# Performance work log

Measured on AMD Instinct MI355X. Metric: run time of the kernel, lower is better.

The kernel has to match this reference:

```python
import jax, jax.numpy as jnp
import numpy as np

B, DEC_T, ENC_T = 64, 128, 1024
H, ENC_D, ATTN, VOCAB = 512, 512, 512, 128


def setup_inputs() -> dict:
    key = jax.random.key(0)
    ks = jax.random.split(key, 12)
    s = 0.05
    return {
        "inputs": jax.random.randint(ks[0], (B, DEC_T), 0, 127),
        "encoder_outputs": jax.random.normal(ks[1], (B, ENC_T, ENC_D), jnp.float32),
        "embedding": jax.random.normal(ks[2], (VOCAB, H), jnp.float32) * s,
        "w_ih": jax.random.normal(ks[3], (3 * H, H + ENC_D), jnp.float32) * s,
        "w_hh": jax.random.normal(ks[4], (3 * H, H), jnp.float32) * s,
        "b_ih": jnp.zeros((3 * H,), jnp.float32),
        "b_hh": jnp.zeros((3 * H,), jnp.float32),
        "attn_wq": jax.random.normal(ks[5], (ATTN, H), jnp.float32) * s,
        "attn_wv": jax.random.normal(ks[6], (ATTN, ENC_D), jnp.float32) * s,
        "attn_conv_w": jax.random.normal(ks[7], (ATTN, 1, 3), jnp.float32) * s,
        "attn_conv_b": jnp.zeros((ATTN,), jnp.float32),
        "attn_bias": jnp.zeros((ATTN,), jnp.float32),
        "attn_v": jax.random.normal(ks[8], (ATTN,), jnp.float32) * s,
        "fc_w": jax.random.normal(ks[9], (VOCAB, H + ENC_D), jnp.float32) * s,
        "fc_b": jnp.zeros((VOCAB,), jnp.float32),
    }


def reference(inputs, encoder_outputs, embedding, w_ih, w_hh, b_ih, b_hh,
              attn_wq, attn_wv, attn_conv_w, attn_conv_b, attn_bias, attn_v,
              fc_w, fc_b):
    emb = embedding[inputs]  # (B, dec_T, H); no eos in inputs so filter is identity
    # precompute encoder value projection once (reused every step)
    enc_proj = jnp.einsum('bte,ae->bta', encoder_outputs, attn_wv)  # (B, enc_T, A)

    def gru_step(h, x):
        gi = x @ w_ih.T + b_ih  # (B, 3H)
        gh = h @ w_hh.T + b_hh
        r = jax.nn.sigmoid(gi[:, :H] + gh[:, :H])
        z = jax.nn.sigmoid(gi[:, H:2 * H] + gh[:, H:2 * H])
        n = jnp.tanh(gi[:, 2 * H:] + r * gh[:, 2 * H:])
        return (1.0 - z) * n + z * h

    def step(carry, x_t):
        h, context, attn_w = carry
        rnn_in = jnp.concatenate([x_t, context], axis=1)  # (B, H+enc_D)
        h = gru_step(h, rnn_in)  # output == new hidden for 1-layer GRU
        # location-aware attention: conv over previous attention weights
        conv = jax.lax.conv_general_dilated(
            attn_w[:, None, :], attn_conv_w, (1,), ((1, 1),),
            dimension_numbers=('NCH', 'OIH', 'NCH'))  # (B, A, enc_T)
        conv_feat = conv.transpose(0, 2, 1) + attn_conv_b  # (B, enc_T, A)
        q = h @ attn_wq.T  # (B, A)
        e = jnp.tanh(q[:, None, :] + enc_proj + conv_feat + attn_bias)
        score = jnp.einsum('bta,a->bt', e, attn_v)  # (B, enc_T)
        attn_w = jax.nn.softmax(score, axis=-1)
        context = jnp.einsum('bt,bte->be', attn_w, encoder_outputs)  # (B, enc_D)
        out_cat = jnp.concatenate([h, context], axis=1)  # (B, H+enc_D)
        pred = jax.nn.log_softmax(out_cat @ fc_w.T + fc_b, axis=-1)  # (B, V)
        return (h, context, attn_w), (pred, attn_w, out_cat)

    init = (jnp.zeros((B, H), emb.dtype),
            jnp.zeros((B, ENC_D), emb.dtype),
            jnp.zeros((B, ENC_T), emb.dtype))
    _, (y, aw, oc) = jax.lax.scan(step, init, emb.transpose(1, 0, 2))
    # back to batch-major: (B, dec_T, *)
    return (y.transpose(1, 0, 2), aw.transpose(1, 0, 2), oc.transpose(1, 0, 2))
```

## Files before the change

### kernel.cpp

```cpp
#include <hip/hip_runtime.h>
#include <stdint.h>

#define BB 64
#define SS 128
#define EE 1024
#define HH 512
#define DD 512
#define AA 512
#define VV 128
#define KX 1536
#define NC 2048

#define AW_OFF ((size_t)BB*SS*VV)
#define OC_OFF (AW_OFF + (size_t)BB*SS*EE)

typedef unsigned short u16;

__device__ __forceinline__ float sigmoid_f(float x){
  return __builtin_amdgcn_rcpf(1.f + __expf(-x));
}
__device__ __forceinline__ float tanh_f(float x){
  float e = __expf(2.f*x);
  return 1.f - 2.f*__builtin_amdgcn_rcpf(e + 1.f);
}
__device__ __forceinline__ u16 f2bf(float f){
  uint32_t u = __float_as_uint(f);
  return (u16)((u + 0x7fffu + ((u>>16)&1u)) >> 16);
}

__global__ void k_build(const float* __restrict__ w_ih, const float* __restrict__ w_hh,
                        const float* __restrict__ b_ih, const float* __restrict__ b_hh,
                        const float* __restrict__ wq,   const float* __restrict__ wv,
                        const float* __restrict__ fc_w,
                        float* __restrict__ Wbig, float* __restrict__ wqT,
                        float* __restrict__ wvT,  float* __restrict__ fcT,
                        float* __restrict__ bias_big){
  int i = blockIdx.x*256 + threadIdx.x;
  const int NW = KX*NC;
  if (i < NW){
    int k = i >> 11, c = i & (NC-1);
    float v;
    if (c < 1024)      v = (k < 1024) ? w_ih[c*1024 + k] : w_hh[c*512 + (k-1024)];
    else if (c < 1536) v = (k < 1024) ? w_ih[c*1024 + k] : 0.f;
    else               v = (k >= 1024) ? w_hh[(c-512)*512 + (k-1024)] : 0.f;
    Wbig[i] = v; return;
  }
  i -= NW;
  if (i < 512*512){ int j = i >> 9, a = i & 511; wqT[i] = wq[a*512 + j]; return; }
  i -= 512*512;
  if (i < 512*512){ int e = i >> 9, a = i & 511; wvT[i] = wv[a*512 + e]; return; }
  i -= 512*512;
  if (i < 1024*128){ int k = i >> 7, v = i & 127; fcT[i] = fc_w[v*1024 + k]; return; }
  i -= 1024*128;
  if (i < NC){
    float bv;
    if (i < 1024)      bv = b_ih[i] + b_hh[i];
    else if (i < 1536) bv = b_ih[i];
    else               bv = b_hh[i - 512];
    bias_big[i] = bv;
  }
}

__global__ __launch_bounds__(256) void k_encp(const float* __restrict__ enc,
                                              const float* __restrict__ wvT,
                                              const float* __restrict__ abias,
                                              const float* __restrict__ convb,
                                              u16* __restrict__ encp){
  __shared__ float As[64][36];
  __shared__ float Bs[32][68];
  int tid = threadIdx.x;
  int r0 = blockIdx.x * 64;
  int a0 = blockIdx.y * 64;
  float4 acc[4];
  #pragma unroll
  for (int r = 0; r < 4; ++r) acc[r] = make_float4(0.f,0.f,0.f,0.f);
  int rl = tid >> 2, kl0 = (tid & 3) * 8;
  int kl2 = tid >> 3, al0 = (tid & 7) * 8;
  int br = (tid >> 4) * 4, cc = (tid & 15) * 4;
  for (int kk = 0; kk < 512; kk += 32){
    float4 av0 = *(const float4*)&enc[(size_t)(r0+rl)*512 + kk + kl0];
    float4 av1 = *(const float4*)&enc[(size_t)(r0+rl)*512 + kk + kl0 + 4];
    float4 bv0 = *(const float4*)&wvT[(size_t)(kk+kl2)*512 + a0 + al0];
    float4 bv1 = *(const float4*)&wvT[(size_t)(kk+kl2)*512 + a0 + al0 + 4];
    __syncthreads();
    *(float4*)&As[rl][kl0]     = av0;
    *(float4*)&As[rl][kl0+4]   = av1;
    *(float4*)&Bs[kl2][al0]    = bv0;
    *(float4*)&Bs[kl2][al0+4]  = bv1;
    __syncthreads();
    #pragma unroll
    for (int i = 0; i < 32; ++i){
      float4 b4 = *(const float4*)&Bs[i][cc];
      float x0 = As[br][i], x1 = As[br+1][i], x2 = As[br+2][i], x3 = As[br+3][i];
      acc[0].x += x0*b4.x; acc[0].y += x0*b4.y; acc[0].z += x0*b4.z; acc[0].w += x0*b4.w;
      acc[1].x += x1*b4.x; acc[1].y += x1*b4.y; acc[1].z += x1*b4.z; acc[1].w += x1*b4.w;
      acc[2].x += x2*b4.x; acc[2].y += x2*b4.y; acc[2].z += x2*b4.z; acc[2].w += x2*b4.w;
      acc[3].x += x3*b4.x; acc[3].y += x3*b4.y; acc[3].z += x3*b4.z; acc[3].w += x3*b4.w;
    }
  }
  int a = a0 + cc;
  float b0f = abias[a]   + convb[a];
  float b1f = abias[a+1] + convb[a+1];
  float b2f_ = abias[a+2] + convb[a+2];
  float b3f = abias[a+3] + convb[a+3];
  #pragma unroll
  for (int r = 0; r < 4; ++r){
    size_t row = (size_t)(r0 + br + r);
    ushort4 pk;
    pk.x = f2bf(acc[r].x + b0f);
    pk.y = f2bf(acc[r].y + b1f);
    pk.z = f2bf(acc[r].z + b2f_);
    pk.w = f2bf(acc[r].w + b3f);
    *(ushort4*)&encp[row*512 + a] = pk;
  }
}

__global__ __launch_bounds__(256) void k_ggemm(const int* __restrict__ inputs,
                                               const float* __restrict__ emb,
                                               const float* __restrict__ ctx,
                                               const float* __restrict__ h,
                                               const float* __restrict__ Wbig,
                                               float* __restrict__ Gp, int s){
  __shared__ float Xs[64][36];
  __shared__ float Ws[32][68];
  int tid = threadIdx.x;
  int c0 = blockIdx.x * 64;
  int kc = blockIdx.y;
  int kbase = kc * 192;
  float4 acc[4];
  #pragma unroll
  for (int r = 0; r < 4; ++r) acc[r] = make_float4(0.f,0.f,0.f,0.f);
  int bl = tid >> 2, kl0 = (tid & 3) * 8;
  int kw = tid >> 3, cl0 = (tid & 7) * 8;
  int br = (tid >> 4) * 4, cc = (tid & 15) * 4;
  const float* emb_b = emb + (size_t)inputs[bl*SS + s]*HH;
  bool t0 = (s == 0);
  for (int kk = 0; kk < 192; kk += 32){
    float xv[8];
    #pragma unroll
    for (int u = 0; u < 8; ++u){
      int kg = kbase + kk + kl0 + u;
      float v;
      if (kg < 512)       v = emb_b[kg];
      else if (kg < 1024) v = t0 ? 0.f : ctx[bl*512 + kg - 512];
      else                v = t0 ? 0.f : h[bl*512 + kg - 1024];
      xv[u] = v;
    }
    float4 w1 = *(const float4*)&Wbig[(size_t)(kbase+kk+kw)*NC + c0 + cl0];
    float4 w2 = *(const float4*)&Wbig[(size_t)(kbase+kk+kw)*NC + c0 + cl0 + 4];
    __syncthreads();
    *(float4*)&Xs[bl][kl0]   = make_float4(xv[0],xv[1],xv[2],xv[3]);
    *(float4*)&Xs[bl][kl0+4] = make_float4(xv[4],xv[5],xv[6],xv[7]);
    *(float4*)&Ws[kw][cl0]   = w1;
    *(float4*)&Ws[kw][cl0+4] = w2;
    __syncthreads();
    #pragma unroll
    for (int i = 0; i < 32; ++i){
      float4 b4 = *(const float4*)&Ws[i][cc];
      float x0 = Xs[br][i], x1 = Xs[br+1][i], x2 = Xs[br+2][i], x3 = Xs[br+3][i];
      acc[0].x += x0*b4.x; acc[0].y += x0*b4.y; acc[0].z += x0*b4.z; acc[0].w += x0*b4.w;
      acc[1].x += x1*b4.x; acc[1].y += x1*b4.y; acc[1].z += x1*b4.z; acc[1].w += x1*b4.w;
      acc[2].x += x2*b4.x; acc[2].y += x2*b4.y; acc[2].z += x2*b4.z; acc[2].w += x2*b4.w;
      acc[3].x += x3*b4.x; acc[3].y += x3*b4.y; acc[3].z += x3*b4.z; acc[3].w += x3*b4.w;
    }
  }
  #pragma unroll
  for (int r = 0; r < 4; ++r)
    *(float4*)&Gp[(size_t)(kc*64 + br + r)*NC + c0 + cc] = acc[r];
}

__global__ __launch_bounds__(256) void k_gate_q(const float* __restrict__ Gp,
                                                const float* __restrict__ bias_big,
                                                float* __restrict__ h,
                                                const float* __restrict__ wqT,
                                                float* __restrict__ qp,
                                                float* __restrict__ out, int s){
  __shared__ float h_l[512];
  int tid = threadIdx.x;
  int jt = blockIdx.x, bt = blockIdx.y;
  bool t0 = (s == 0);
  #pragma unroll
  for (int it = 0; it < 2; ++it){
    int item = tid + it*256;
    int bi = item >> 6, jl = item & 63;
    int b = bt*8 + bi, j = jt*64 + jl;
    float s0=0.f, s1=0.f, s2=0.f, s3=0.f;
    #pragma unroll
    for (int kc = 0; kc < 8; ++kc){
      const float* g = Gp + (size_t)(kc*64 + b)*NC;
      s0 += g[j]; s1 += g[512+j]; s2 += g[1024+j]; s3 += g[1536+j];
    }
    float r = sigmoid_f(s0 + bias_big[j]);
    float z = sigmoid_f(s1 + bias_big[512+j]);
    float n = tanh_f(s2 + bias_big[1024+j] + r*(s3 + bias_big[1536+j]));
    float hold = t0 ? 0.f : h[b*512 + j];
    float hn = (1.f - z)*n + z*hold;
    h_l[item] = hn;
    h[b*512 + j] = hn;
    out[OC_OFF + (size_t)(b*SS + s)*1024 + j] = hn;
  }
  __syncthreads();
  int a0 = tid*2;
  float2 acc8[8];
  #pragma unroll
  for (int bi = 0; bi < 8; ++bi) acc8[bi] = make_float2(0.f, 0.f);
  for (int j = 0; j < 64; ++j){
    float2 w = *(const float2*)&wqT[(size_t)(jt*64 + j)*512 + a0];
    #pragma unroll
    for (int bi = 0; bi < 8; ++bi){
      float hv = h_l[bi*64 + j];
      acc8[bi].x += hv*w.x; acc8[bi].y += hv*w.y;
    }
  }
  #pragma unroll
  for (int bi = 0; bi < 8; ++bi)
    *(float2*)&qp[(size_t)(jt*64 + bt*8 + bi)*512 + a0] = acc8[bi];
}

__global__ __launch_bounds__(1024) void k_score(const float* __restrict__ qp,
                                                const float* __restrict__ attn_v,
                                                const float* __restrict__ conv_w,
                                                const u16* __restrict__ encp,
                                                const float* __restrict__ out_aw,
                                                float* __restrict__ score, int s){
  __shared__ float q_l[512], v_l[512], c0_l[512], c1_l[512], c2_l[512];
  int tid = threadIdx.x;
  int b = blockIdx.y, et = blockIdx.x;
  if (tid < 512){
    float qq = 0.f;
    #pragma unroll
    for (int jt = 0; jt < 8; ++jt) qq += qp[(size_t)(jt*64 + b)*512 + tid];
    q_l[tid]  = qq;
    v_l[tid]  = attn_v[tid];
    c0_l[tid] = conv_w[tid*3 + 0];
    c1_l[tid] = conv_w[tid*3 + 1];
    c2_l[tid] = conv_w[tid*3 + 2];
  }
  __syncthreads();
  int wave = tid >> 6, lane = tid & 63;
  float q8[8], v8[8], c08[8], c18[8], c28[8];
  #pragma unroll
  for (int i = 0; i < 8; ++i){
    int a = lane*8 + i;
    q8[i] = q_l[a]; v8[i] = v_l[a]; c08[i] = c0_l[a]; c18[i] = c1_l[a]; c28[i] = c2_l[a];
  }
  const float* awrow = out_aw + AW_OFF + (size_t)(b*SS + (s-1))*EE;
  #pragma unroll
  for (int eu = 0; eu < 8; ++eu){
    int e = et*128 + wave*8 + eu;
    float wl = 0.f, wc = 0.f, wr = 0.f;
    if (s > 0){
      wc = awrow[e];
      wl = (e > 0)    ? awrow[e-1] : 0.f;
      wr = (e < EE-1) ? awrow[e+1] : 0.f;
    }
    uint4 pk = *(const uint4*)(encp + ((size_t)(b*EE + e)*512 + lane*8));
    uint32_t ua[4] = {pk.x, pk.y, pk.z, pk.w};
    float acc = 0.f;
    #pragma unroll
    for (int p = 0; p < 4; ++p){
      float plo = __uint_as_float(ua[p] << 16);
      float phi = __uint_as_float(ua[p] & 0xffff0000u);
      int i = p*2;
      float v0 = q8[i]   + plo + c08[i]*wl   + c18[i]*wc   + c28[i]*wr;
      acc += tanh_f(v0) * v8[i];
      float v1 = q8[i+1] + phi + c08[i+1]*wl + c18[i+1]*wc + c28[i+1]*wr;
      acc += tanh_f(v1) * v8[i+1];
    }
    #pragma unroll
    for (int off = 32; off; off >>= 1) acc += __shfl_xor(acc, off, 64);
    if (lane == 0) score[b*EE + e] = acc;
  }
}

__global__ __launch_bounds__(256) void k_soft_ctx(const float* __restrict__ score,
                                                  const float* __restrict__ enc,
                                                  float* __restrict__ ctxp,
                                                  float* __restrict__ out, int s){
  __shared__ float s_l[1024];
  __shared__ float red[256];
  __shared__ float w_l[128];
  int tid = threadIdx.x;
  int c = blockIdx.x, b = blockIdx.y;
  float lv[4];
  #pragma unroll
  for (int u = 0; u < 4; ++u){
    lv[u] = score[b*EE + u*256 + tid];
    s_l[u*256 + tid] = lv[u];
  }
  float m = fmaxf(fmaxf(lv[0], lv[1]), fmaxf(lv[2], lv[3]));
  red[tid] = m; __syncthreads();
  for (int st = 128; st > 0; st >>= 1){
    if (tid < st) red[tid] = fmaxf(red[tid], red[tid+st]);
    __syncthreads();
  }
  m = red[0]; __syncthreads();
  float sm = 0.f;
  #pragma unroll
  for (int u = 0; u < 4; ++u) sm += __expf(lv[u] - m);
  red[tid] = sm; __syncthreads();
  for (int st = 128; st > 0; st >>= 1){
    if (tid < st) red[tid] += red[tid+st];
    __syncthreads();
  }
  float rS = __builtin_amdgcn_rcpf(red[0]);
  if (tid < 128){
    int e = c*128 + tid;
    float w = __expf(s_l[e] - m) * rS;
    w_l[tid] = w;
    out[AW_OFF + (size_t)(b*SS + s)*EE + e] = w;
  }
  __syncthreads();
  int d0 = tid*2;
  float a0 = 0.f, a1 = 0.f;
  for (int i = 0; i < 128; ++i){
    float2 ev = *(const float2*)&enc[((size_t)b*EE + c*128 + i)*512 + d0];
    float w = w_l[i];
    a0 += w*ev.x; a1 += w*ev.y;
  }
  *(float2*)&ctxp[(size_t)(c*64 + b)*512 + d0] = make_float2(a0, a1);
}

__global__ __launch_bounds__(256) void k_fc(const float* __restrict__ h,
                                            const float* __restrict__ ctxp,
                                            float* __restrict__ ctx,
                                            const float* __restrict__ fcT,
                                            const float* __restrict__ fc_b,
                                            float* __restrict__ out, int s){
  __shared__ float oc_l[1024];
  __shared__ float lp[2][128];
  __shared__ float l_l[128];
  int tid = threadIdx.x, b = blockIdx.x;
  oc_l[tid]       = h[b*512 + tid];
  oc_l[tid + 256] = h[b*512 + tid + 256];
  int d0 = tid*2;
  float a0 = 0.f, a1 = 0.f;
  #pragma unroll
  for (int cc = 0; cc < 8; ++cc){
    float2 p = *(const float2*)&ctxp[(size_t)(cc*64 + b)*512 + d0];
    a0 += p.x; a1 += p.y;
  }
  oc_l[512 + d0]     = a0;
  oc_l[512 + d0 + 1] = a1;
  ctx[b*512 + d0]     = a0;
  ctx[b*512 + d0 + 1] = a1;
  size_t oco = OC_OFF + (size_t)(b*SS + s)*1024 + 512 + d0;
  out[oco]     = a0;
  out[oco + 1] = a1;
  __syncthreads();
  int v = tid & 127, half = tid >> 7;
  float acc = 0.f;
  #pragma unroll 8
  for (int k = 0; k < 512; ++k)
    acc += oc_l[half*512 + k] * fcT[(size_t)(half*512 + k)*128 + v];
  lp[half][v] = acc;
  __syncthreads();
  if (tid < 128) l_l[tid] = lp[0][tid] + lp[1][tid] + fc_b[tid];
  __syncthreads();
  if (tid < 128){
    float m = -1e30f;
    for (int i = 0; i < 128; ++i) m = fmaxf(m, l_l[i]);
    float sm = 0.f;
    for (int i = 0; i < 128; ++i) sm += __expf(l_l[i] - m);
    out[(size_t)(b*SS + s)*VV + tid] = l_l[tid] - m - __logf(sm);
  }
}

extern "C" void kernel_launch(void* const* d_in, const int* in_sizes, int n_in,
                              void* d_out, int out_size, void* d_ws, size_t ws_size,
                              hipStream_t stream){
  (void)in_sizes; (void)n_in; (void)out_size; (void)ws_size;
  const int*   inputs = (const int*)d_in[0];
  const float* enc    = (const float*)d_in[1];
  const float* emb    = (const float*)d_in[2];
  const float* w_ih   = (const float*)d_in[3];
  const float* w_hh   = (const float*)d_in[4];
  const float* b_ih   = (const float*)d_in[5];
  const float* b_hh   = (const float*)d_in[6];
  const float* wq     = (const float*)d_in[7];
  const float* wv     = (const float*)d_in[8];
  const float* convw  = (const float*)d_in[9];
  const float* convb  = (const float*)d_in[10];
  const float* abias  = (const float*)d_in[11];
  const float* av     = (const float*)d_in[12];
  const float* fcw    = (const float*)d_in[13];
  const float* fcb    = (const float*)d_in[14];
  float* out = (float*)d_out;

  char* p = (char*)d_ws;
  auto alloc = [&](size_t bytes)->char*{
    char* r = p; p += (bytes + 255) & ~(size_t)255; return r;
  };
  u16*   encp  = (u16*)  alloc((size_t)BB*EE*AA*2);
  float* Wbig  = (float*)alloc((size_t)KX*NC*4);
  float* wqT   = (float*)alloc((size_t)512*512*4);
  float* wvT   = (float*)alloc((size_t)512*512*4);
  float* fcT   = (float*)alloc((size_t)1024*128*4);
  float* biasb = (float*)alloc((size_t)NC*4);
  float* hbuf  = (float*)alloc((size_t)BB*HH*4);
  float* ctx   = (float*)alloc((size_t)BB*DD*4);
  float* Gp    = (float*)alloc((size_t)8*BB*NC*4);
  float* qp    = (float*)alloc((size_t)8*BB*AA*4);
  float* score = (float*)alloc((size_t)BB*EE*4);
  float* ctxp  = (float*)alloc((size_t)8*BB*DD*4);

  int total0 = KX*NC + 512*512 + 512*512 + 1024*128 + NC;
  k_build<<<(total0 + 255)/256, 256, 0, stream>>>(w_ih, w_hh, b_ih, b_hh, wq, wv, fcw,
                                                  Wbig, wqT, wvT, fcT, biasb);
  k_encp<<<dim3(1024, 8), 256, 0, stream>>>(enc, wvT, abias, convb, encp);

  for (int s = 0; s < SS; ++s){
    k_ggemm<<<dim3(32, 8), 256, 0, stream>>>(inputs, emb, ctx, hbuf, Wbig, Gp, s);
    k_gate_q<<<dim3(8, 8), 256, 0, stream>>>(Gp, biasb, hbuf, wqT, qp, out, s);
    k_score<<<dim3(8, 64), 1024, 0, stream>>>(qp, av, convw, encp, out, score, s);
    k_soft_ctx<<<dim3(8, 64), 256, 0, stream>>>(score, enc, ctxp, out, s);
    k_fc<<<64, 256, 0, stream>>>(hbuf, ctxp, ctx, fcT, fcb, out, s);
  }
}
```

Measured before the change: 11.54 ms.

## Fuse FC into next step's gate GEMM and read encoder in bf16

```diff
diff --git a/kernel.cpp b/kernel.cpp
--- a/kernel.cpp
+++ b/kernel.cpp
@@ -115,58 +115,118 @@
   }
 }
 
-__global__ __launch_bounds__(256) void k_ggemm(const int* __restrict__ inputs,
-                                               const float* __restrict__ emb,
-                                               const float* __restrict__ ctx,
-                                               const float* __restrict__ h,
-                                               const float* __restrict__ Wbig,
-                                               float* __restrict__ Gp, int s){
-  __shared__ float Xs[64][36];
-  __shared__ float Ws[32][68];
+__global__ __launch_bounds__(256) void k_encbf(const float* __restrict__ enc,
+                                               u16* __restrict__ enc_bf){
+  size_t i = ((size_t)blockIdx.x*256 + threadIdx.x) * 4;
+  float4 v = *(const float4*)&enc[i];
+  ushort4 pk;
+  pk.x = f2bf(v.x); pk.y = f2bf(v.y); pk.z = f2bf(v.z); pk.w = f2bf(v.w);
+  *(ushort4*)&enc_bf[i] = pk;
+}
+
+__global__ __launch_bounds__(256) void k_ggemm_fc(const int* __restrict__ inputs,
+                                                  const float* __restrict__ emb,
+                                                  const float* __restrict__ ctxp,
+                                                  const float* __restrict__ h,
+                                                  const float* __restrict__ Wbig,
+                                                  float* __restrict__ Gp,
+                                                  const float* __restrict__ fcT,
+                                                  const float* __restrict__ fc_b,
+                                                  float* __restrict__ out,
+                                                  int s, int gemm_nb, int sfc){
   int tid = threadIdx.x;
-  int c0 = blockIdx.x * 64;
-  int kc = blockIdx.y;
-  int kbase = kc * 192;
-  float4 acc[4];
-  #pragma unroll
-  for (int r = 0; r < 4; ++r) acc[r] = make_float4(0.f,0.f,0.f,0.f);
-  int bl = tid >> 2, kl0 = (tid & 3) * 8;
-  int kw = tid >> 3, cl0 = (tid & 7) * 8;
-  int br = (tid >> 4) * 4, cc = (tid & 15) * 4;
-  const float* emb_b = emb + (size_t)inputs[bl*SS + s]*HH;
-  bool t0 = (s == 0);
-  for (int kk = 0; kk < 192; kk += 32){
-    float xv[8];
-    #pragma unroll
-    for (int u = 0; u < 8; ++u){
-      int kg = kbase + kk + kl0 + u;
-      float v;
-      if (kg < 512)       v = emb_b[kg];
-      else if (kg < 1024) v = t0 ? 0.f : ctx[bl*512 + kg - 512];
-      else                v = t0 ? 0.f : h[bl*512 + kg - 1024];
-      xv[u] = v;
-    }
-    float4 w1 = *(const float4*)&Wbig[(size_t)(kbase+kk+kw)*NC + c0 + cl0];
-    float4 w2 = *(const float4*)&Wbig[(size_t)(kbase+kk+kw)*NC + c0 + cl0 + 4];
-    __syncthreads();
-    *(float4*)&Xs[bl][kl0]   = make_float4(xv[0],xv[1],xv[2],xv[3]);
-    *(float4*)&Xs[bl][kl0+4] = make_float4(xv[4],xv[5],xv[6],xv[7]);
-    *(float4*)&Ws[kw][cl0]   = w1;
-    *(float4*)&Ws[kw][cl0+4] = w2;
-    __syncthreads();
-    #pragma unroll
-    for (int i = 0; i < 32; ++i){
-      float4 b4 = *(const float4*)&Ws[i][cc];
-      float x0 = Xs[br][i], x1 = Xs[br+1][i], x2 = Xs[br+2][i], x3 = Xs[br+3][i];
-      acc[0].x += x0*b4.x; acc[0].y += x0*b4.y; acc[0].z += x0*b4.z; acc[0].w += x0*b4.w;
-      acc[1].x += x1*b4.x; acc[1].y += x1*b4.y; acc[1].z += x1*b4.z; acc[1].w += x1*b4.w;
-      acc[2].x += x2*b4.x; acc[2].y += x2*b4.y; acc[2].z += x2*b4.z; acc[2].w += x2*b4.w;
-      acc[3].x += x3*b4.x; acc[3].y += x3*b4.y; acc[3].z += x3*b4.z; acc[3].w += x3*b4.w;
-    }
-  }
-  #pragma unroll
-  for (int r = 0; r < 4; ++r)
-    *(float4*)&Gp[(size_t)(kc*64 + br + r)*NC + c0 + cc] = acc[r];
+  if ((int)blockIdx.x < gemm_nb){
+    __shared__ float Xs[64][36];
+    __shared__ float Ws[32][68];
+    int bid = blockIdx.x;
+    int c0 = (bid & 31) * 64;
+    int kc = bid >> 5;
+    int kbase = kc * 192;
+    float4 acc[4];
+    #pragma unroll
+    for (int r = 0; r < 4; ++r) acc[r] = make_float4(0.f,0.f,0.f,0.f);
+    int bl = tid >> 2, kl0 = (tid & 3) * 8;
+    int kw = tid >> 3, cl0 = (tid & 7) * 8;
+    int br = (tid >> 4) * 4, cc = (tid & 15) * 4;
+    const float* emb_b = emb + (size_t)inputs[bl*SS + s]*HH;
+    bool t0 = (s == 0);
+    for (int kk = 0; kk < 192; kk += 32){
+      float xv[8];
+      #pragma unroll
+      for (int u = 0; u < 8; ++u){
+        int kg = kbase + kk + kl0 + u;
+        float v;
+        if (kg < 512)       v = emb_b[kg];
+        else if (kg < 1024){
+          if (t0) v = 0.f;
+          else {
+            int d = kg - 512;
+            v = ctxp[(size_t)(0*64+bl)*512 + d] + ctxp[(size_t)(1*64+bl)*512 + d]
+              + ctxp[(size_t)(2*64+bl)*512 + d] + ctxp[(size_t)(3*64+bl)*512 + d];
+          }
+        }
+        else                v = t0 ? 0.f : h[bl*512 + kg - 1024];
+        xv[u] = v;
+      }
+      float4 w1 = *(const float4*)&Wbig[(size_t)(kbase+kk+kw)*NC + c0 + cl0];
+      float4 w2 = *(const float4*)&Wbig[(size_t)(kbase+kk+kw)*NC + c0 + cl0 + 4];
+      __syncthreads();
+      *(float4*)&Xs[bl][kl0]   = make_float4(xv[0],xv[1],xv[2],xv[3]);
+      *(float4*)&Xs[bl][kl0+4] = make_float4(xv[4],xv[5],xv[6],xv[7]);
+      *(float4*)&Ws[kw][cl0]   = w1;
+      *(float4*)&Ws[kw][cl0+4] = w2;
+      __syncthreads();
+      #pragma unroll
+      for (int i = 0; i < 32; ++i){
+        float4 b4 = *(const float4*)&Ws[i][cc];
+        float x0 = Xs[br][i], x1 = Xs[br+1][i], x2 = Xs[br+2][i], x3 = Xs[br+3][i];
+        acc[0].x += x0*b4.x; acc[0].y += x0*b4.y; acc[0].z += x0*b4.z; acc[0].w += x0*b4.w;
+        acc[1].x += x1*b4.x; acc[1].y += x1*b4.y; acc[1].z += x1*b4.z; acc[1].w += x1*b4.w;
+        acc[2].x += x2*b4.x; acc[2].y += x2*b4.y; acc[2].z += x2*b4.z; acc[2].w += x2*b4.w;
+        acc[3].x += x3*b4.x; acc[3].y += x3*b4.y; acc[3].z += x3*b4.z; acc[3].w += x3*b4.w;
+      }
+    }
+    #pragma unroll
+    for (int r = 0; r < 4; ++r)
+      *(float4*)&Gp[(size_t)(kc*64 + br + r)*NC + c0 + cc] = acc[r];
+  } else {
+    if (sfc < 0) return;
+    __shared__ float oc_l[1024];
+    __shared__ float lp[2][128];
+    __shared__ float l_l[128];
+    int b = blockIdx.x - gemm_nb;
+    oc_l[tid]       = h[b*512 + tid];
+    oc_l[tid + 256] = h[b*512 + tid + 256];
+    int d0 = tid*2;
+    float a0 = 0.f, a1 = 0.f;
+    #pragma unroll
+    for (int cc2 = 0; cc2 < 4; ++cc2){
+      float2 p2 = *(const float2*)&ctxp[(size_t)(cc2*64 + b)*512 + d0];
+      a0 += p2.x; a1 += p2.y;
+    }
+    oc_l[512 + d0]     = a0;
+    oc_l[512 + d0 + 1] = a1;
+    size_t oco = OC_OFF + (size_t)(b*SS + sfc)*1024 + 512 + d0;
+    out[oco]     = a0;
+    out[oco + 1] = a1;
+    __syncthreads();
+    int v = tid & 127, half = tid >> 7;
+    float acc = 0.f;
+    #pragma unroll 8
+    for (int k = 0; k < 512; ++k)
+      acc += oc_l[half*512 + k] * fcT[(size_t)(half*512 + k)*128 + v];
+    lp[half][v] = acc;
+    __syncthreads();
+    if (tid < 128) l_l[tid] = lp[0][tid] + lp[1][tid] + fc_b[tid];
+    __syncthreads();
+    if (tid < 128){
+      float m = -1e30f;
+      for (int i = 0; i < 128; ++i) m = fmaxf(m, l_l[i]);
+      float sm = 0.f;
+      for (int i = 0; i < 128; ++i) sm += __expf(l_l[i] - m);
+      out[(size_t)(b*SS + sfc)*VV + tid] = l_l[tid] - m - __logf(sm);
+    }
+  }
 }
 
 __global__ __launch_bounds__(256) void k_gate_q(const float* __restrict__ Gp,
@@ -273,96 +333,70 @@
   }
 }
 
-__global__ __launch_bounds__(256) void k_soft_ctx(const float* __restrict__ score,
-                                                  const float* __restrict__ enc,
+__global__ __launch_bounds__(512) void k_soft_ctx(const float* __restrict__ score,
+                                                  const u16* __restrict__ enc_bf,
                                                   float* __restrict__ ctxp,
                                                   float* __restrict__ out, int s){
   __shared__ float s_l[1024];
-  __shared__ float red[256];
-  __shared__ float w_l[128];
+  __shared__ float red[512];
+  __shared__ float w_l[256];
+  __shared__ float redc[8][512];
   int tid = threadIdx.x;
   int c = blockIdx.x, b = blockIdx.y;
-  float lv[4];
-  #pragma unroll
-  for (int u = 0; u < 4; ++u){
-    lv[u] = score[b*EE + u*256 + tid];
-    s_l[u*256 + tid] = lv[u];
-  }
-  float m = fmaxf(fmaxf(lv[0], lv[1]), fmaxf(lv[2], lv[3]));
+  float lv0 = score[b*EE + tid];
+  float lv1 = score[b*EE + 512 + tid];
+  s_l[tid] = lv0; s_l[512 + tid] = lv1;
+  float m = fmaxf(lv0, lv1);
   red[tid] = m; __syncthreads();
-  for (int st = 128; st > 0; st >>= 1){
+  for (int st = 256; st > 0; st >>= 1){
     if (tid < st) red[tid] = fmaxf(red[tid], red[tid+st]);
     __syncthreads();
   }
   m = red[0]; __syncthreads();
-  float sm = 0.f;
-  #pragma unroll
-  for (int u = 0; u < 4; ++u) sm += __expf(lv[u] - m);
+  float sm = __expf(lv0 - m) + __expf(lv1 - m);
   red[tid] = sm; __syncthreads();
-  for (int st = 128; st > 0; st >>= 1){
+  for (int st = 256; st > 0; st >>= 1){
     if (tid < st) red[tid] += red[tid+st];
     __syncthreads();
   }
   float rS = __builtin_amdgcn_rcpf(red[0]);
-  if (tid < 128){
-    int e = c*128 + tid;
+  if (tid < 256){
+    int e = c*256 + tid;
     float w = __expf(s_l[e] - m) * rS;
     w_l[tid] = w;
     out[AW_OFF + (size_t)(b*SS + s)*EE + e] = w;
   }
   __syncthreads();
-  int d0 = tid*2;
-  float a0 = 0.f, a1 = 0.f;
-  for (int i = 0; i < 128; ++i){
-    float2 ev = *(const float2*)&enc[((size_t)b*EE + c*128 + i)*512 + d0];
-    float w = w_l[i];
-    a0 += w*ev.x; a1 += w*ev.y;
-  }
-  *(float2*)&ctxp[(size_t)(c*64 + b)*512 + d0] = make_float2(a0, a1);
-}
-
-__global__ __launch_bounds__(256) void k_fc(const float* __restrict__ h,
-                                            const float* __restrict__ ctxp,
-                                            float* __restrict__ ctx,
-                                            const float* __restrict__ fcT,
-                                            const float* __restrict__ fc_b,
-                                            float* __restrict__ out, int s){
-  __shared__ float oc_l[1024];
-  __shared__ float lp[2][128];
-  __shared__ float l_l[128];
-  int tid = threadIdx.x, b = blockIdx.x;
-  oc_l[tid]       = h[b*512 + tid];
-  oc_l[tid + 256] = h[b*512 + tid + 256];
-  int d0 = tid*2;
-  float a0 = 0.f, a1 = 0.f;
-  #pragma unroll
-  for (int cc = 0; cc < 8; ++cc){
-    float2 p = *(const float2*)&ctxp[(size_t)(cc*64 + b)*512 + d0];
-    a0 += p.x; a1 += p.y;
-  }
-  oc_l[512 + d0]     = a0;
-  oc_l[512 + d0 + 1] = a1;
-  ctx[b*512 + d0]     = a0;
-  ctx[b*512 + d0 + 1] = a1;
-  size_t oco = OC_OFF + (size_t)(b*SS + s)*1024 + 512 + d0;
-  out[oco]     = a0;
-  out[oco + 1] = a1;
-  __syncthreads();
-  int v = tid & 127, half = tid >> 7;
-  float acc = 0.f;
-  #pragma unroll 8
-  for (int k = 0; k < 512; ++k)
-    acc += oc_l[half*512 + k] * fcT[(size_t)(half*512 + k)*128 + v];
-  lp[half][v] = acc;
-  __syncthreads();
-  if (tid < 128) l_l[tid] = lp[0][tid] + lp[1][tid] + fc_b[tid];
+  int es = tid >> 6, lane = tid & 63;
+  int d0 = lane * 8;
+  float acc8[8];
+  #pragma unroll
+  for (int i = 0; i < 8; ++i) acc8[i] = 0.f;
+  #pragma unroll 4
+  for (int i = 0; i < 32; ++i){
+    int e_loc = es*32 + i;
+    int e = c*256 + e_loc;
+    uint4 pk = *(const uint4*)(enc_bf + ((size_t)b*EE + e)*512 + d0);
+    float w = w_l[e_loc];
+    uint32_t ua[4] = {pk.x, pk.y, pk.z, pk.w};
+    #pragma unroll
+    for (int p = 0; p < 4; ++p){
+      acc8[p*2]   += w * __uint_as_float(ua[p] << 16);
+      acc8[p*2+1] += w * __uint_as_float(ua[p] & 0xffff0000u);
+    }
+  }
+  #pragma unroll
+  for (int i = 0; i < 8; ++i) redc[es][d0 + i] = acc8[i];
   __syncthreads();
   if (tid < 128){
-    float m = -1e30f;
-    for (int i = 0; i < 128; ++i) m = fmaxf(m, l_l[i]);
-    float sm = 0.f;
-    for (int i = 0; i < 128; ++i) sm += __expf(l_l[i] - m);
-    out[(size_t)(b*SS + s)*VV + tid] = l_l[tid] - m - __logf(sm);
+    int d = tid * 4;
+    float4 t = make_float4(0.f,0.f,0.f,0.f);
+    #pragma unroll
+    for (int e2 = 0; e2 < 8; ++e2){
+      float4 r4 = *(const float4*)&redc[e2][d];
+      t.x += r4.x; t.y += r4.y; t.z += r4.z; t.w += r4.w;
+    }
+    *(float4*)&ctxp[(size_t)(c*64 + b)*512 + d] = t;
   }
 }
 
@@ -391,29 +425,34 @@
   auto alloc = [&](size_t bytes)->char*{
     char* r = p; p += (bytes + 255) & ~(size_t)255; return r;
   };
-  u16*   encp  = (u16*)  alloc((size_t)BB*EE*AA*2);
-  float* Wbig  = (float*)alloc((size_t)KX*NC*4);
-  float* wqT   = (float*)alloc((size_t)512*512*4);
-  float* wvT   = (float*)alloc((size_t)512*512*4);
-  float* fcT   = (float*)alloc((size_t)1024*128*4);
-  float* biasb = (float*)alloc((size_t)NC*4);
-  float* hbuf  = (float*)alloc((size_t)BB*HH*4);
-  float* ctx   = (float*)alloc((size_t)BB*DD*4);
-  float* Gp    = (float*)alloc((size_t)8*BB*NC*4);
-  float* qp    = (float*)alloc((size_t)8*BB*AA*4);
-  float* score = (float*)alloc((size_t)BB*EE*4);
-  float* ctxp  = (float*)alloc((size_t)8*BB*DD*4);
+  u16*   encp   = (u16*)  alloc((size_t)BB*EE*AA*2);
+  u16*   enc_bf = (u16*)  alloc((size_t)BB*EE*DD*2);
+  float* Wbig   = (float*)alloc((size_t)KX*NC*4);
+  float* wqT    = (float*)alloc((size_t)512*512*4);
+  float* wvT    = (float*)alloc((size_t)512*512*4);
+  float* fcT    = (float*)alloc((size_t)1024*128*4);
+  float* biasb  = (float*)alloc((size_t)NC*4);
+  float* hbuf   = (float*)alloc((size_t)BB*HH*4);
+  float* Gp     = (float*)alloc((size_t)8*BB*NC*4);
+  float* qp     = (float*)alloc((size_t)8*BB*AA*4);
+  float* score  = (float*)alloc((size_t)BB*EE*4);
+  float* ctxp   = (float*)alloc((size_t)4*BB*DD*4);
 
   int total0 = KX*NC + 512*512 + 512*512 + 1024*128 + NC;
   k_build<<<(total0 + 255)/256, 256, 0, stream>>>(w_ih, w_hh, b_ih, b_hh, wq, wv, fcw,
                                                   Wbig, wqT, wvT, fcT, biasb);
   k_encp<<<dim3(1024, 8), 256, 0, stream>>>(enc, wvT, abias, convb, encp);
+  k_encbf<<<(BB*EE*DD/4 + 255)/256, 256, 0, stream>>>(enc, enc_bf);
 
   for (int s = 0; s < SS; ++s){
-    k_ggemm<<<dim3(32, 8), 256, 0, stream>>>(inputs, emb, ctx, hbuf, Wbig, Gp, s);
+    int sfc = s - 1;
+    int grid = (sfc >= 0) ? 320 : 256;
+    k_ggemm_fc<<<grid, 256, 0, stream>>>(inputs, emb, ctxp, hbuf, Wbig, Gp,
+                                         fcT, fcb, out, s, 256, sfc);
     k_gate_q<<<dim3(8, 8), 256, 0, stream>>>(Gp, biasb, hbuf, wqT, qp, out, s);
     k_score<<<dim3(8, 64), 1024, 0, stream>>>(qp, av, convw, encp, out, score, s);
-    k_soft_ctx<<<dim3(8, 64), 256, 0, stream>>>(score, enc, ctxp, out, s);
-    k_fc<<<64, 256, 0, stream>>>(hbuf, ctxp, ctx, fcT, fcb, out, s);
-  }
-}
+    k_soft_ctx<<<dim3(4, 64), 512, 0, stream>>>(score, enc_bf, ctxp, out, s);
+  }
+  k_ggemm_fc<<<64, 256, 0, stream>>>(inputs, emb, ctxp, hbuf, Wbig, Gp,
+                                     fcT, fcb, out, 0, 0, SS-1);
+}
```

After: 10.04 ms. 1.15x faster.
